# Kernel optimization log

Hardware: AMD Instinct MI355X
Metric: run time of the kernel (lower is better)

## Reference

```python
import jax, jax.numpy as jnp
import numpy as np

B, S, D, E, H, K = 2, 2048, 1024, 8, 2048, 2
EM_ITERS = 5
LB_WEIGHT = 0.1
EPS = 1e-8


def setup_inputs() -> dict:
    key = jax.random.key(0)
    ks = jax.random.split(key, 12)
    sc = 0.02
    return {
        "x": jax.random.normal(ks[0], (B, S, D), jnp.float32),
        "gate_W": jax.random.normal(ks[1], (D, E), jnp.float32) * sc,
        "gate_b": jnp.zeros((E,), jnp.float32),
        "gate_temp": jnp.ones((1,), jnp.float32),
        "W1": jax.random.normal(ks[2], (E, D, H), jnp.float32) * sc,
        "b1": jnp.zeros((E, H), jnp.float32),
        "W2": jax.random.normal(ks[3], (E, H, D), jnp.float32) * sc,
        "b2": jnp.zeros((E, D), jnp.float32),
        "sW1": jax.random.normal(ks[4], (D, H), jnp.float32) * sc,
        "sb1": jnp.zeros((H,), jnp.float32),
        "sW2": jax.random.normal(ks[5], (H, D), jnp.float32) * sc,
        "sb2": jnp.zeros((D,), jnp.float32),
    }


def reference(x, gate_W, gate_b, gate_temp, W1, b1, W2, b2, sW1, sb1, sW2, sb2):
    Bq, Sq, Dq = x.shape
    T = Bq * Sq
    xf = x.reshape(T, Dq)  # (T, D)

    # Router: gate linear + learned temperature
    gate_logits = xf @ gate_W + gate_b              # (T, E)
    tempered = gate_logits / gate_temp               # (T, E)
    expert_weights = jax.nn.softmax(tempered, axis=-1)
    _, topk_idx = jax.lax.top_k(expert_weights, K)   # (T, K) int32
    first = topk_idx[:, 0]

    # Load-balance loss: KL(uniform || empirical top-1 usage) (fresh counters)
    usage = jnp.zeros((E,), jnp.float32).at[first].add(1.0)
    actual = usage / jnp.float32(T)
    actual = actual + EPS
    actual = actual / actual.sum()
    u = jnp.float32(1.0 / E)
    kl = jnp.sum(u * (jnp.log(u) - jnp.log(actual)))
    load_balance_loss = LB_WEIGHT * kl

    # EM expert-load reweighting on tempered logits
    scores = jax.nn.softmax(tempered, axis=-1)       # (T, E)
    p = jnp.full((E,), 1.0 / E, jnp.float32)
    for _ in range(EM_ITERS):
        ea = scores * p                               # (T, E)
        ea = ea / (ea.sum(axis=-1, keepdims=True) + EPS)
        counts = ea.sum(axis=0)                       # (E,)
        p = counts / (counts.sum() + EPS)
    balanced = scores * p                             # (T, E)

    # All-expert FFN (dense, equivalent to per-expert masked compute)
    h = jax.nn.relu(jnp.einsum('td,edh->teh', xf, W1) + b1)  # (T, E, H)
    eo = jnp.einsum('teh,ehd->ted', h, W2) + b2              # (T, E, D)

    # Combine top-k experts with balanced weights
    w_k = jnp.take_along_axis(balanced, topk_idx, axis=1)        # (T, K)
    out_k = jnp.take_along_axis(eo, topk_idx[:, :, None], axis=1)  # (T, K, D)
    out = jnp.einsum('tk,tkd->td', w_k, out_k)                   # (T, D)

    # Shared expert, weighted by 0.1
    shared = jax.nn.relu(xf @ sW1 + sb1) @ sW2 + sb2
    out = out + 0.1 * shared

    return out.reshape(Bq, Sq, Dq), load_balance_loss
```

## Files before the change

### kernel.cpp

```cpp
#include <hip/hip_runtime.h>
#include <math.h>

#define T_TOK 4096
#define D_DIM 1024
#define H_DIM 2048
#define NE 8
#define EPSF 1e-8f
#define G1_GEMM 448
#define G2_GEMM 224
#define NTR128 1152

typedef __attribute__((ext_vector_type(8))) short bf16x8;
typedef __attribute__((ext_vector_type(4))) float f32x4;

__device__ __forceinline__ unsigned short f2bf(float f) {
  unsigned u = __float_as_uint(f);
  u += 0x7fffu + ((u >> 16) & 1u);
  return (unsigned short)(u >> 16);
}

__device__ __forceinline__ void gload_lds16(const void* g, void* l) {
  __builtin_amdgcn_global_load_lds(
      (const __attribute__((address_space(1))) unsigned int*)g,
      (__attribute__((address_space(3))) unsigned int*)l, 16, 0, 0);
}

#define WAITV(n) asm volatile("s_waitcnt vmcnt(" #n ")" ::: "memory")
#define BARR()                                  \
  do {                                          \
    asm volatile("" ::: "memory");              \
    __builtin_amdgcn_s_barrier();               \
    asm volatile("" ::: "memory");              \
  } while (0)

__device__ __forceinline__ void transpose_tile128(const float* __restrict__ src,
                                                  unsigned short* __restrict__ dst,
                                                  int R, int C, int r0, int c0, int tid,
                                                  float* tile) {
#pragma unroll
  for (int k = 0; k < 8; ++k) {
    int id = tid + k * 512;
    int row = id >> 5, c4 = (id & 31) * 4;
    float4 v = *(const float4*)(src + (size_t)(r0 + row) * C + c0 + c4);
    float* tr = tile + row * 129 + c4;
    tr[0] = v.x; tr[1] = v.y; tr[2] = v.z; tr[3] = v.w;
  }
  __syncthreads();
#pragma unroll
  for (int k = 0; k < 4; ++k) {
    int id = tid + k * 512;
    int oc = id >> 4;
    int rbase = (id & 15) * 8;
    uint4 wv;
    unsigned* wp = (unsigned*)&wv;
#pragma unroll
    for (int j = 0; j < 4; ++j) {
      unsigned lo = f2bf(tile[(rbase + 2 * j) * 129 + oc]);
      unsigned hi = f2bf(tile[(rbase + 2 * j + 1) * 129 + oc]);
      wp[j] = lo | (hi << 16);
    }
    *(uint4*)(dst + (size_t)(c0 + oc) * R + r0 + rbase) = wv;
  }
}

__global__ __launch_bounds__(512, 4) void gate_kernel(
    const float* __restrict__ x, const float* __restrict__ gW, const float* __restrict__ gb,
    const float* __restrict__ gtemp, unsigned short* __restrict__ xb,
    float* __restrict__ scores, int* __restrict__ idx,
    unsigned* __restrict__ usage, unsigned* __restrict__ cnt, int* __restrict__ perm) {
  __shared__ float gWl[D_DIM * 9];
  __shared__ int toks[16];
  int tid = threadIdx.x, wave = tid >> 6, lane = tid & 63;
  int t0 = blockIdx.x * 8;

#pragma unroll
  for (int k = 0; k < 4; ++k) {
    int q = tid + k * 512;
    float4 f = ((const float4*)gW)[q];
    int d = q >> 1, eo = (q & 1) * 4;
    float* dst = &gWl[d * 9 + eo];
    dst[0] = f.x; dst[1] = f.y; dst[2] = f.z; dst[3] = f.w;
  }
  __syncthreads();

  int t = t0 + wave;
  const float* xr = x + (size_t)t * D_DIM;
  unsigned short* xbr = xb + (size_t)t * D_DIM;
  float part[NE];
#pragma unroll
  for (int e = 0; e < NE; ++e) part[e] = 0.f;
#pragma unroll
  for (int i = 0; i < 16; ++i) {
    int d = lane + 64 * i;
    float xv = xr[d];
    xbr[d] = f2bf(xv);
    const float* g = &gWl[d * 9];
#pragma unroll
    for (int e = 0; e < NE; ++e) part[e] += xv * g[e];
  }
#pragma unroll
  for (int e = 0; e < NE; ++e) {
    float v = part[e];
    for (int off = 32; off; off >>= 1) v += __shfl_xor(v, off);
    part[e] = v;
  }
  float temp = gtemp[0];
  float mx = -1e30f;
#pragma unroll
  for (int e = 0; e < NE; ++e) { part[e] = (part[e] + gb[e]) / temp; mx = fmaxf(mx, part[e]); }
  float s = 0.f;
#pragma unroll
  for (int e = 0; e < NE; ++e) { part[e] = expf(part[e] - mx); s += part[e]; }
  float inv = 1.0f / s;
#pragma unroll
  for (int e = 0; e < NE; ++e) part[e] *= inv;
  if (lane == 0) {
    float4* sp = (float4*)(scores + (size_t)t * NE);
    sp[0] = make_float4(part[0], part[1], part[2], part[3]);
    sp[1] = make_float4(part[4], part[5], part[6], part[7]);
    int i0 = 0; float b0 = part[0];
#pragma unroll
    for (int e = 1; e < NE; ++e) if (part[e] > b0) { b0 = part[e]; i0 = e; }
    int i1 = -1; float b1 = -1e30f;
#pragma unroll
    for (int e = 0; e < NE; ++e) if (e != i0 && part[e] > b1) { b1 = part[e]; i1 = e; }
    idx[t * 2] = i0; idx[t * 2 + 1] = i1;
    toks[wave * 2] = i0; toks[wave * 2 + 1] = i1;
  }
  __syncthreads();
  if (tid < NE) {
    int c0 = 0, c1 = 0;
#pragma unroll
    for (int j = 0; j < 8; ++j) {
      if (toks[j * 2] == tid) ++c0;
      if (toks[j * 2 + 1] == tid) ++c1;
    }
    if (c0) atomicAdd(&usage[tid], (unsigned)c0);
    int tot = c0 + c1;
    if (tot) {
      unsigned b = atomicAdd(&cnt[tid], (unsigned)tot);
      int p = 0;
#pragma unroll
      for (int j = 0; j < 8; ++j) {
        if (toks[j * 2] == tid) perm[(size_t)tid * T_TOK + b + p++] = (t0 + j) * 2;
        if (toks[j * 2 + 1] == tid) perm[(size_t)tid * T_TOK + b + p++] = (t0 + j) * 2 + 1;
      }
    }
  }
}

__global__ __launch_bounds__(512) void transW1_kernel(
    const float* __restrict__ W1, const float* __restrict__ sW1,
    unsigned short* __restrict__ W1t, unsigned short* __restrict__ sW1t) {
  __shared__ float tile[128 * 129];
  int l = blockIdx.x;
  int m = l >> 7, rem = l & 127;
  int c0 = (rem & 15) * 128, r0 = (rem >> 4) * 128;
  const float* src = (m < NE) ? W1 + (size_t)m * D_DIM * H_DIM : sW1;
  unsigned short* dst = (m < NE) ? W1t + (size_t)m * D_DIM * H_DIM : sW1t;
  transpose_tile128(src, dst, D_DIM, H_DIM, r0, c0, threadIdx.x, tile);
}

__device__ __forceinline__ void em_block512(const float* __restrict__ scores,
                                            const unsigned* __restrict__ usage,
                                            float* __restrict__ p_out, float* __restrict__ loss_out,
                                            int tid, char* smem) {
  float* p_sh = (float*)smem;
  float* cw = p_sh + 8;
  float* counts_sh = cw + 64;
  int wave = tid >> 6, lane = tid & 63;
  float s[8][NE];
#pragma unroll
  for (int rr = 0; rr < 8; ++rr) {
    int row = tid + rr * 512;
    const float4* sp = (const float4*)(scores + (size_t)row * NE);
    float4 a = sp[0], b = sp[1];
    s[rr][0] = a.x; s[rr][1] = a.y; s[rr][2] = a.z; s[rr][3] = a.w;
    s[rr][4] = b.x; s[rr][5] = b.y; s[rr][6] = b.z; s[rr][7] = b.w;
  }
  if (tid < NE) p_sh[tid] = 1.0f / NE;
  __syncthreads();
  for (int it = 0; it < 5; ++it) {
    float p[NE];
#pragma unroll
    for (int e = 0; e < NE; ++e) p[e] = p_sh[e];
    float c[NE];
#pragma unroll
    for (int e = 0; e < NE; ++e) c[e] = 0.f;
#pragma unroll
    for (int rr = 0; rr < 8; ++rr) {
      float denom = 0.f;
#pragma unroll
      for (int e = 0; e < NE; ++e) denom += s[rr][e] * p[e];
      float inv = 1.0f / (denom + EPSF);
#pragma unroll
      for (int e = 0; e < NE; ++e) c[e] += s[rr][e] * p[e] * inv;
    }
#pragma unroll
    for (int e = 0; e < NE; ++e) {
      float v = c[e];
      for (int off = 32; off; off >>= 1) v += __shfl_xor(v, off);
      c[e] = v;
    }
    if (lane == 0) {
#pragma unroll
      for (int e = 0; e < NE; ++e) cw[wave * 8 + e] = c[e];
    }
    __syncthreads();
    if (tid < NE) {
      float tot = 0.f;
#pragma unroll
      for (int w = 0; w < 8; ++w) tot += cw[w * 8 + tid];
      counts_sh[tid] = tot;
    }
    __syncthreads();
    if (tid < NE) {
      float total = 0.f;
#pragma unroll
      for (int e = 0; e < NE; ++e) total += counts_sh[e];
      p_sh[tid] = counts_sh[tid] / (total + EPSF);
    }
    __syncthreads();
  }
  if (tid < NE) p_out[tid] = p_sh[tid];
  if (tid == 0) {
    float actual[NE]; float norm = 0.f;
#pragma unroll
    for (int e = 0; e < NE; ++e) { actual[e] = (float)usage[e] / (float)T_TOK + EPSF; norm += actual[e]; }
    float u = 1.0f / NE;
    float kl = 0.f;
#pragma unroll
    for (int e = 0; e < NE; ++e) kl += u * (logf(u) - logf(actual[e] / norm));
    loss_out[0] = 0.1f * kl;
  }
}

template <int KDIM, int NDIM, bool RELU, bool MODE1>
__device__ __forceinline__ void gemm_body(
    unsigned short* lds, int flat,
    const unsigned short* __restrict__ A, const unsigned short* __restrict__ WE,
    const unsigned short* __restrict__ WS, const float* __restrict__ biasE,
    const float* __restrict__ biasS, const int* __restrict__ perm,
    const unsigned* __restrict__ cnt, void* __restrict__ outp) {
  constexpr int BM = 256, BN = 256, BK = 64;
  constexpr int NT = NDIM / BN;
  constexpr int NKT = KDIM / BK;

  int tc[9];
#pragma unroll
  for (int i = 0; i < NE; ++i) tc[i] = ((int)cnt[i] + 255) >> 8;
  tc[8] = T_TOK / 256;
  int nt = 0;
#pragma unroll
  for (int i = 0; i < 9; ++i) nt += tc[i];
  int W = nt * NT;
  int xcd = flat & 7, pos = flat >> 3;
  int q = W >> 3, r = W & 7;
  int mycount = q + (xcd < r ? 1 : 0);
  if (pos >= mycount) return;
  int mystart = xcd * q + (xcd < r ? xcd : r);
  int w = mystart + pos;
  int ti = w / NT;
  int n0 = (w % NT) * BN;
  int e = 0, mt = ti;
  while (mt >= tc[e]) { mt -= tc[e]; ++e; }
  int m0 = mt * BM;
  int cnt_e = (e == NE) ? T_TOK : (int)cnt[e];

  const unsigned short* Bmat = (e == NE) ? WS : WE + (size_t)e * KDIM * NDIM;
  const float* bias = (e == NE) ? biasS : biasE + (size_t)e * NDIM;

  int tid = threadIdx.x, wave = tid >> 6, lane = tid & 63;
  int wm = wave >> 1, wn = wave & 1;
  int frow = lane & 15, fks = lane >> 4;

  int srow = wave * 8 + (lane >> 3);
  int sslot = lane & 7;
  const unsigned short* aptr[2][2];
  const unsigned short* bptr[2][2];
#pragma unroll
  for (int h = 0; h < 2; ++h)
#pragma unroll
    for (int j = 0; j < 2; ++j) {
      int rr = h * 128 + j * 64 + srow;
      int colsw = (sslot ^ (rr & 7)) << 3;
      int ar = m0 + rr;
      if (ar > cnt_e - 1) ar = cnt_e - 1;
      int gar;
      if (e == NE) gar = MODE1 ? ar : (2 * T_TOK + ar);
      else { int v = perm[(size_t)e * T_TOK + ar]; gar = MODE1 ? (v >> 1) : v; }
      aptr[h][j] = A + (size_t)gar * KDIM + colsw;
      bptr[h][j] = Bmat + (size_t)(n0 + rr) * KDIM + colsw;
    }

  auto stA = [&](int t, int h) {
    int dbe = (t & 1) * 16384;
    int k0 = t * BK;
    gload_lds16(aptr[h][0] + k0, &lds[dbe + h * 8192 + wave * 512]);
    gload_lds16(aptr[h][1] + k0, &lds[dbe + h * 8192 + wave * 512 + 4096]);
  };
  auto stB = [&](int t, int h) {
    int dbe = (t & 1) * 16384;
    int k0 = t * BK;
    gload_lds16(bptr[h][0] + k0, &lds[32768 + dbe + h * 8192 + wave * 512]);
    gload_lds16(bptr[h][1] + k0, &lds[32768 + dbe + h * 8192 + wave * 512 + 4096]);
  };

  auto rdA = [&](int dbe, int ks, int m) -> bf16x8 {
    int rr = wm * 64 + m * 16 + frow;
    int slot = (ks * 4 + fks) ^ (rr & 7);
    return *(const bf16x8*)&lds[dbe + rr * 64 + slot * 8];
  };
  auto rdB = [&](int dbe, int ks, int bh, int jj) -> bf16x8 {
    int rr = bh * 128 + jj * 32 + wn * 16 + frow;
    int slot = (ks * 4 + fks) ^ (rr & 7);
    return *(const bf16x8*)&lds[32768 + dbe + rr * 64 + slot * 8];
  };

  f32x4 acc[4][8];
#pragma unroll
  for (int m = 0; m < 4; ++m)
#pragma unroll
    for (int nn = 0; nn < 8; ++nn) acc[m][nn] = (f32x4){0.f, 0.f, 0.f, 0.f};

  stA(0, 0); stA(0, 1);
  stB(0, 0); stB(0, 1);
  stA(1, 0); stA(1, 1);
  WAITV(6);
  BARR();

  for (int t = 0; t < NKT; ++t) {
    const int dbe = (t & 1) * 16384;
    bf16x8 a0[4], a1[4], bfr[4];

#pragma unroll
    for (int m = 0; m < 4; ++m) a0[m] = rdA(dbe, 0, m);
#pragma unroll
    for (int jj = 0; jj < 4; ++jj) bfr[jj] = rdB(dbe, 0, 0, jj);
    if (t + 1 < NKT) stB(t + 1, 0);
    BARR();
    __builtin_amdgcn_s_setprio(1);
#pragma unroll
    for (int m = 0; m < 4; ++m)
#pragma unroll
      for (int jj = 0; jj < 4; ++jj)
        acc[m][jj] = __builtin_amdgcn_mfma_f32_16x16x32_bf16(a0[m], bfr[jj], acc[m][jj], 0, 0, 0);
    __builtin_amdgcn_s_setprio(0);
    BARR();

#pragma unroll
    for (int m = 0; m < 4; ++m) a1[m] = rdA(dbe, 1, m);
#pragma unroll
    for (int jj = 0; jj < 4; ++jj) bfr[jj] = rdB(dbe, 1, 0, jj);
    if (t + 1 < NKT) stB(t + 1, 1);
    BARR();
    __builtin_amdgcn_s_setprio(1);
#pragma unroll
    for (int m = 0; m < 4; ++m)
#pragma unroll
      for (int jj = 0; jj < 4; ++jj)
        acc[m][jj] = __builtin_amdgcn_mfma_f32_16x16x32_bf16(a1[m], bfr[jj], acc[m][jj], 0, 0, 0);
    __builtin_amdgcn_s_setprio(0);
    if (t + 1 < NKT) { WAITV(8); } else { WAITV(0); }
    BARR();

#pragma unroll
    for (int jj = 0; jj < 4; ++jj) bfr[jj] = rdB(dbe, 0, 1, jj);
    if (t + 2 < NKT) stA(t + 2, 0);
    BARR();
    __builtin_amdgcn_s_setprio(1);
#pragma unroll
    for (int m = 0; m < 4; ++m)
#pragma unroll
      for (int jj = 0; jj < 4; ++jj)
        acc[m][4 + jj] = __builtin_amdgcn_mfma_f32_16x16x32_bf16(a0[m], bfr[jj], acc[m][4 + jj], 0, 0, 0);
    __builtin_amdgcn_s_setprio(0);
    BARR();

#pragma unroll
    for (int jj = 0; jj < 4; ++jj) bfr[jj] = rdB(dbe, 1, 1, jj);
    if (t + 2 < NKT) stA(t + 2, 1);
    BARR();
    __builtin_amdgcn_s_setprio(1);
#pragma unroll
    for (int m = 0; m < 4; ++m)
#pragma unroll
      for (int jj = 0; jj < 4; ++jj)
        acc[m][4 + jj] = __builtin_amdgcn_mfma_f32_16x16x32_bf16(a1[m], bfr[jj], acc[m][4 + jj], 0, 0, 0);
    __builtin_amdgcn_s_setprio(0);
    if (t + 1 < NKT) {
      if (t + 2 < NKT) { WAITV(6); } else { WAITV(2); }
    }
    BARR();
  }

#pragma unroll
  for (int m = 0; m < 4; ++m) {
#pragma unroll
    for (int qq = 0; qq < 4; ++qq) {
      int rt = wm * 64 + m * 16 + (lane >> 4) * 4 + qq;
      if (m0 + rt >= cnt_e) continue;
      int rr;
      if (e == NE) rr = 2 * T_TOK + m0 + rt;
      else rr = perm[(size_t)e * T_TOK + m0 + rt];
#pragma unroll
      for (int nn = 0; nn < 8; ++nn) {
        int col = n0 + (nn >> 2) * 128 + (nn & 3) * 32 + wn * 16 + (lane & 15);
        float val = acc[m][nn][qq] + bias[col];
        if (RELU) val = fmaxf(val, 0.f);
        if (MODE1)
          ((unsigned short*)outp)[(size_t)rr * NDIM + col] = f2bf(val);
        else
          ((float*)outp)[(size_t)rr * NDIM + col] = val;
      }
    }
  }
}

__global__ __launch_bounds__(512, 2) void gemm1_kernel(
    const unsigned short* __restrict__ xb, const unsigned short* __restrict__ W1t,
    const unsigned short* __restrict__ sW1t, const float* __restrict__ b1,
    const float* __restrict__ sb1, const int* __restrict__ perm, const unsigned* __restrict__ cnt,
    unsigned short* __restrict__ Hbuf,
    const float* __restrict__ W2, const float* __restrict__ sW2,
    unsigned short* __restrict__ W2t, unsigned short* __restrict__ sW2t,
    const float* __restrict__ scores, const unsigned* __restrict__ usage,
    float* __restrict__ pbuf, float* __restrict__ loss_out) {
  __shared__ char smem[131072];
  int flat = blockIdx.x;
  if (flat < G1_GEMM) {
    gemm_body<D_DIM, H_DIM, true, true>((unsigned short*)smem, flat, xb, W1t, sW1t, b1, sb1,
                                        perm, cnt, (void*)Hbuf);
    return;
  }
  int l = flat - G1_GEMM;
  if (l < NTR128) {
    int m = l >> 7, rem = l & 127;
    int c0 = (rem & 7) * 128, r0 = (rem >> 3) * 128;
    const float* src = (m < NE) ? W2 + (size_t)m * H_DIM * D_DIM : sW2;
    unsigned short* dst = (m < NE) ? W2t + (size_t)m * H_DIM * D_DIM : sW2t;
    transpose_tile128(src, dst, H_DIM, D_DIM, r0, c0, threadIdx.x, (float*)smem);
    return;
  }
  em_block512(scores, usage, pbuf, loss_out, threadIdx.x, smem);
}

template <int KDIM, int NDIM, bool RELU, bool MODE1>
__global__ __launch_bounds__(512, 2) void gemm_kernel(
    const unsigned short* __restrict__ A, const unsigned short* __restrict__ WE,
    const unsigned short* __restrict__ WS, const float* __restrict__ biasE,
    const float* __restrict__ biasS, const int* __restrict__ perm,
    const unsigned* __restrict__ cnt, void* __restrict__ outp) {
  __shared__ char smem[131072];
  gemm_body<KDIM, NDIM, RELU, MODE1>((unsigned short*)smem, blockIdx.x, A, WE, WS, biasE, biasS,
                                     perm, cnt, outp);
}

__global__ void combine_kernel(const float* __restrict__ ebuf, const float* __restrict__ scores,
                               const float* __restrict__ p, const int* __restrict__ idx,
                               float* __restrict__ out) {
  int gid = blockIdx.x * blockDim.x + threadIdx.x;
  int t = gid >> 8;
  int d4 = gid & 255;
  int e0 = idx[t * 2], e1 = idx[t * 2 + 1];
  float w0 = scores[(size_t)t * NE + e0] * p[e0];
  float w1 = scores[(size_t)t * NE + e1] * p[e1];
  const float4* r0 = (const float4*)(ebuf + (size_t)(t * 2) * D_DIM);
  const float4* r1 = (const float4*)(ebuf + (size_t)(t * 2 + 1) * D_DIM);
  const float4* rs = (const float4*)(ebuf + (size_t)(2 * T_TOK + t) * D_DIM);
  float4 a = r0[d4], b = r1[d4], c = rs[d4];
  float4 o;
  o.x = w0 * a.x + w1 * b.x + 0.1f * c.x;
  o.y = w0 * a.y + w1 * b.y + 0.1f * c.y;
  o.z = w0 * a.z + w1 * b.z + 0.1f * c.z;
  o.w = w0 * a.w + w1 * b.w + 0.1f * c.w;
  ((float4*)out)[gid] = o;
}

extern "C" void kernel_launch(void* const* d_in, const int* in_sizes, int n_in,
                              void* d_out, int out_size, void* d_ws, size_t ws_size,
                              hipStream_t stream) {
  const float* x     = (const float*)d_in[0];
  const float* gW    = (const float*)d_in[1];
  const float* gb    = (const float*)d_in[2];
  const float* gtemp = (const float*)d_in[3];
  const float* W1    = (const float*)d_in[4];
  const float* b1    = (const float*)d_in[5];
  const float* W2    = (const float*)d_in[6];
  const float* b2    = (const float*)d_in[7];
  const float* sW1   = (const float*)d_in[8];
  const float* sb1   = (const float*)d_in[9];
  const float* sW2   = (const float*)d_in[10];
  const float* sb2   = (const float*)d_in[11];
  float* out = (float*)d_out;

  char* ws = (char*)d_ws;
  size_t off = 0;
  auto take = [&](size_t b) { char* ptr = ws + off; off += (b + 255) & ~(size_t)255; return ptr; };
  unsigned short* xb   = (unsigned short*)take((size_t)T_TOK * D_DIM * 2);
  unsigned short* W1t  = (unsigned short*)take((size_t)NE * H_DIM * D_DIM * 2);
  unsigned short* sW1t = (unsigned short*)take((size_t)H_DIM * D_DIM * 2);
  unsigned short* W2t  = (unsigned short*)take((size_t)NE * D_DIM * H_DIM * 2);
  unsigned short* sW2t = (unsigned short*)take((size_t)D_DIM * H_DIM * 2);
  unsigned short* Hbuf = (unsigned short*)take((size_t)3 * T_TOK * H_DIM * 2);
  float* ebuf          = (float*)take((size_t)3 * T_TOK * D_DIM * 4);
  float* scores        = (float*)take((size_t)T_TOK * NE * 4);
  int* idx             = (int*)take((size_t)T_TOK * 2 * 4);
  int* perm            = (int*)take((size_t)NE * T_TOK * 4);
  unsigned* cnt        = (unsigned*)take(256);
  unsigned* usage      = (unsigned*)take(256);
  float* pbuf          = (float*)take(256);
  (void)n_in; (void)in_sizes; (void)out_size; (void)ws_size;

  hipMemsetAsync(cnt, 0, 512, stream);
  gate_kernel<<<512, 512, 0, stream>>>(x, gW, gb, gtemp, xb, scores, idx, usage, cnt, perm);
  transW1_kernel<<<NTR128, 512, 0, stream>>>(W1, sW1, W1t, sW1t);
  gemm1_kernel<<<G1_GEMM + NTR128 + 1, 512, 0, stream>>>(
      xb, W1t, sW1t, b1, sb1, perm, cnt, Hbuf, W2, sW2, W2t, sW2t, scores, usage, pbuf,
      out + (size_t)T_TOK * D_DIM);
  gemm_kernel<H_DIM, D_DIM, false, false><<<G2_GEMM, 512, 0, stream>>>(
      Hbuf, W2t, sW2t, b2, sb2, perm, cnt, (void*)ebuf);
  combine_kernel<<<(T_TOK * D_DIM / 4) / 256, 256, 0, stream>>>(ebuf, scores, pbuf, idx, out);
}
```

Baseline: 198.0 us.

## Shrink GEMM tiles to 256x128x32 with triple-buffered A and fuse gate with W1 transpose

```diff
diff --git a/kernel.cpp b/kernel.cpp
--- a/kernel.cpp
+++ b/kernel.cpp
@@ -6,8 +6,8 @@
 #define H_DIM 2048
 #define NE 8
 #define EPSF 1e-8f
-#define G1_GEMM 448
-#define G2_GEMM 224
+#define G1_GEMM 896
+#define G2_GEMM 448
 #define NTR128 1152
 
 typedef __attribute__((ext_vector_type(8))) short bf16x8;
@@ -63,26 +63,36 @@
   }
 }
 
-__global__ __launch_bounds__(512, 4) void gate_kernel(
+__global__ __launch_bounds__(512, 4) void prep2_kernel(
     const float* __restrict__ x, const float* __restrict__ gW, const float* __restrict__ gb,
-    const float* __restrict__ gtemp, unsigned short* __restrict__ xb,
-    float* __restrict__ scores, int* __restrict__ idx,
+    const float* __restrict__ gtemp, const float* __restrict__ W1, const float* __restrict__ sW1,
+    unsigned short* __restrict__ W1t, unsigned short* __restrict__ sW1t,
+    unsigned short* __restrict__ xb, float* __restrict__ scores, int* __restrict__ idx,
     unsigned* __restrict__ usage, unsigned* __restrict__ cnt, int* __restrict__ perm) {
-  __shared__ float gWl[D_DIM * 9];
-  __shared__ int toks[16];
-  int tid = threadIdx.x, wave = tid >> 6, lane = tid & 63;
-  int t0 = blockIdx.x * 8;
-
+  __shared__ char psm[67584];
+  int b = blockIdx.x, tid = threadIdx.x;
+  if (b >= 512) {
+    int l = b - 512;
+    int m = l >> 7, rem = l & 127;
+    int c0 = (rem & 15) * 128, r0 = (rem >> 4) * 128;
+    const float* src = (m < NE) ? W1 + (size_t)m * D_DIM * H_DIM : sW1;
+    unsigned short* dst = (m < NE) ? W1t + (size_t)m * D_DIM * H_DIM : sW1t;
+    transpose_tile128(src, dst, D_DIM, H_DIM, r0, c0, tid, (float*)psm);
+    return;
+  }
+  float* gWl = (float*)psm;
+  int* toks = (int*)(psm + 36864);
+  int wave = tid >> 6, lane = tid & 63;
+  int t0 = b * 8;
 #pragma unroll
   for (int k = 0; k < 4; ++k) {
     int q = tid + k * 512;
     float4 f = ((const float4*)gW)[q];
     int d = q >> 1, eo = (q & 1) * 4;
-    float* dst = &gWl[d * 9 + eo];
-    dst[0] = f.x; dst[1] = f.y; dst[2] = f.z; dst[3] = f.w;
+    float* dstv = &gWl[d * 9 + eo];
+    dstv[0] = f.x; dstv[1] = f.y; dstv[2] = f.z; dstv[3] = f.w;
   }
   __syncthreads();
-
   int t = t0 + wave;
   const float* xr = x + (size_t)t * D_DIM;
   unsigned short* xbr = xb + (size_t)t * D_DIM;
@@ -138,27 +148,15 @@
     if (c0) atomicAdd(&usage[tid], (unsigned)c0);
     int tot = c0 + c1;
     if (tot) {
-      unsigned b = atomicAdd(&cnt[tid], (unsigned)tot);
+      unsigned bb = atomicAdd(&cnt[tid], (unsigned)tot);
       int p = 0;
 #pragma unroll
       for (int j = 0; j < 8; ++j) {
-        if (toks[j * 2] == tid) perm[(size_t)tid * T_TOK + b + p++] = (t0 + j) * 2;
-        if (toks[j * 2 + 1] == tid) perm[(size_t)tid * T_TOK + b + p++] = (t0 + j) * 2 + 1;
+        if (toks[j * 2] == tid) perm[(size_t)tid * T_TOK + bb + p++] = (t0 + j) * 2;
+        if (toks[j * 2 + 1] == tid) perm[(size_t)tid * T_TOK + bb + p++] = (t0 + j) * 2 + 1;
       }
     }
   }
-}
-
-__global__ __launch_bounds__(512) void transW1_kernel(
-    const float* __restrict__ W1, const float* __restrict__ sW1,
-    unsigned short* __restrict__ W1t, unsigned short* __restrict__ sW1t) {
-  __shared__ float tile[128 * 129];
-  int l = blockIdx.x;
-  int m = l >> 7, rem = l & 127;
-  int c0 = (rem & 15) * 128, r0 = (rem >> 4) * 128;
-  const float* src = (m < NE) ? W1 + (size_t)m * D_DIM * H_DIM : sW1;
-  unsigned short* dst = (m < NE) ? W1t + (size_t)m * D_DIM * H_DIM : sW1t;
-  transpose_tile128(src, dst, D_DIM, H_DIM, r0, c0, threadIdx.x, tile);
 }
 
 __device__ __forceinline__ void em_block512(const float* __restrict__ scores,
@@ -242,7 +240,7 @@
     const unsigned short* __restrict__ WS, const float* __restrict__ biasE,
     const float* __restrict__ biasS, const int* __restrict__ perm,
     const unsigned* __restrict__ cnt, void* __restrict__ outp) {
-  constexpr int BM = 256, BN = 256, BK = 64;
+  constexpr int BM = 256, BN = 128, BK = 32;
   constexpr int NT = NDIM / BN;
   constexpr int NKT = KDIM / BK;
 
@@ -274,124 +272,75 @@
   int wm = wave >> 1, wn = wave & 1;
   int frow = lane & 15, fks = lane >> 4;
 
-  int srow = wave * 8 + (lane >> 3);
-  int sslot = lane & 7;
-  const unsigned short* aptr[2][2];
-  const unsigned short* bptr[2][2];
-#pragma unroll
-  for (int h = 0; h < 2; ++h)
-#pragma unroll
-    for (int j = 0; j < 2; ++j) {
-      int rr = h * 128 + j * 64 + srow;
-      int colsw = (sslot ^ (rr & 7)) << 3;
-      int ar = m0 + rr;
-      if (ar > cnt_e - 1) ar = cnt_e - 1;
-      int gar;
-      if (e == NE) gar = MODE1 ? ar : (2 * T_TOK + ar);
-      else { int v = perm[(size_t)e * T_TOK + ar]; gar = MODE1 ? (v >> 1) : v; }
-      aptr[h][j] = A + (size_t)gar * KDIM + colsw;
-      bptr[h][j] = Bmat + (size_t)(n0 + rr) * KDIM + colsw;
-    }
-
-  auto stA = [&](int t, int h) {
-    int dbe = (t & 1) * 16384;
-    int k0 = t * BK;
-    gload_lds16(aptr[h][0] + k0, &lds[dbe + h * 8192 + wave * 512]);
-    gload_lds16(aptr[h][1] + k0, &lds[dbe + h * 8192 + wave * 512 + 4096]);
+  auto garf = [&](int rrow) {
+    int ar = m0 + rrow; if (ar > cnt_e - 1) ar = cnt_e - 1;
+    int gar;
+    if (e == NE) gar = MODE1 ? ar : (2 * T_TOK + ar);
+    else { int v = perm[(size_t)e * T_TOK + ar]; gar = MODE1 ? (v >> 1) : v; }
+    return gar;
   };
-  auto stB = [&](int t, int h) {
-    int dbe = (t & 1) * 16384;
-    int k0 = t * BK;
-    gload_lds16(bptr[h][0] + k0, &lds[32768 + dbe + h * 8192 + wave * 512]);
-    gload_lds16(bptr[h][1] + k0, &lds[32768 + dbe + h * 8192 + wave * 512 + 4096]);
+  int r0a = wave * 16 + (lane >> 2);
+  int r1a = 128 + wave * 16 + (lane >> 2);
+  int rb = wave * 16 + (lane >> 2);
+  int g0 = (r0a & 3) ^ ((r0a >> 2) & 3);
+  int g1 = (r1a & 3) ^ ((r1a >> 2) & 3);
+  int gbv = (rb & 3) ^ ((rb >> 2) & 3);
+  const unsigned short* aptr0 = A + (size_t)garf(r0a) * KDIM + (((lane & 3) ^ g0) << 3);
+  const unsigned short* aptr1 = A + (size_t)garf(r1a) * KDIM + (((lane & 3) ^ g1) << 3);
+  const unsigned short* bptr = Bmat + (size_t)(n0 + rb) * KDIM + (((lane & 3) ^ gbv) << 3);
+
+  auto stA = [&](int t, int ab) {
+    gload_lds16(aptr0 + t * BK, &lds[ab * 8192 + wave * 512]);
+    gload_lds16(aptr1 + t * BK, &lds[ab * 8192 + 4096 + wave * 512]);
   };
-
-  auto rdA = [&](int dbe, int ks, int m) -> bf16x8 {
+  auto stB = [&](int t) {
+    gload_lds16(bptr + t * BK, &lds[24576 + (t & 1) * 4096 + wave * 512]);
+  };
+
+  auto rdA = [&](int ab, int m) -> bf16x8 {
     int rr = wm * 64 + m * 16 + frow;
-    int slot = (ks * 4 + fks) ^ (rr & 7);
-    return *(const bf16x8*)&lds[dbe + rr * 64 + slot * 8];
+    int sp = fks ^ ((rr & 3) ^ ((rr >> 2) & 3));
+    return *(const bf16x8*)&lds[ab * 8192 + rr * 32 + sp * 8];
   };
-  auto rdB = [&](int dbe, int ks, int bh, int jj) -> bf16x8 {
-    int rr = bh * 128 + jj * 32 + wn * 16 + frow;
-    int slot = (ks * 4 + fks) ^ (rr & 7);
-    return *(const bf16x8*)&lds[32768 + dbe + rr * 64 + slot * 8];
+  auto rdB = [&](int bb, int j) -> bf16x8 {
+    int rr = wn * 64 + j * 16 + frow;
+    int sp = fks ^ ((rr & 3) ^ ((rr >> 2) & 3));
+    return *(const bf16x8*)&lds[24576 + bb * 4096 + rr * 32 + sp * 8];
   };
 
-  f32x4 acc[4][8];
+  f32x4 acc[4][4];
 #pragma unroll
   for (int m = 0; m < 4; ++m)
 #pragma unroll
-    for (int nn = 0; nn < 8; ++nn) acc[m][nn] = (f32x4){0.f, 0.f, 0.f, 0.f};
-
-  stA(0, 0); stA(0, 1);
-  stB(0, 0); stB(0, 1);
-  stA(1, 0); stA(1, 1);
-  WAITV(6);
+    for (int j = 0; j < 4; ++j) acc[m][j] = (f32x4){0.f, 0.f, 0.f, 0.f};
+
+  stA(0, 0); stB(0); stA(1, 1);
+  WAITV(2);
   BARR();
 
+  int ab = 0;
   for (int t = 0; t < NKT; ++t) {
-    const int dbe = (t & 1) * 16384;
-    bf16x8 a0[4], a1[4], bfr[4];
-
-#pragma unroll
-    for (int m = 0; m < 4; ++m) a0[m] = rdA(dbe, 0, m);
-#pragma unroll
-    for (int jj = 0; jj < 4; ++jj) bfr[jj] = rdB(dbe, 0, 0, jj);
-    if (t + 1 < NKT) stB(t + 1, 0);
+    int bb = t & 1;
+    bf16x8 a[4], b[4];
+#pragma unroll
+    for (int m = 0; m < 4; ++m) a[m] = rdA(ab, m);
+#pragma unroll
+    for (int j = 0; j < 4; ++j) b[j] = rdB(bb, j);
+    if (t + 1 < NKT) stB(t + 1);
+    if (t + 2 < NKT) { int ab2 = ab + 2; if (ab2 >= 3) ab2 -= 3; stA(t + 2, ab2); }
     BARR();
     __builtin_amdgcn_s_setprio(1);
 #pragma unroll
     for (int m = 0; m < 4; ++m)
 #pragma unroll
-      for (int jj = 0; jj < 4; ++jj)
-        acc[m][jj] = __builtin_amdgcn_mfma_f32_16x16x32_bf16(a0[m], bfr[jj], acc[m][jj], 0, 0, 0);
-    __builtin_amdgcn_s_setprio(0);
-    BARR();
-
-#pragma unroll
-    for (int m = 0; m < 4; ++m) a1[m] = rdA(dbe, 1, m);
-#pragma unroll
-    for (int jj = 0; jj < 4; ++jj) bfr[jj] = rdB(dbe, 1, 0, jj);
-    if (t + 1 < NKT) stB(t + 1, 1);
-    BARR();
-    __builtin_amdgcn_s_setprio(1);
-#pragma unroll
-    for (int m = 0; m < 4; ++m)
-#pragma unroll
-      for (int jj = 0; jj < 4; ++jj)
-        acc[m][jj] = __builtin_amdgcn_mfma_f32_16x16x32_bf16(a1[m], bfr[jj], acc[m][jj], 0, 0, 0);
-    __builtin_amdgcn_s_setprio(0);
-    if (t + 1 < NKT) { WAITV(8); } else { WAITV(0); }
-    BARR();
-
-#pragma unroll
-    for (int jj = 0; jj < 4; ++jj) bfr[jj] = rdB(dbe, 0, 1, jj);
-    if (t + 2 < NKT) stA(t + 2, 0);
-    BARR();
-    __builtin_amdgcn_s_setprio(1);
-#pragma unroll
-    for (int m = 0; m < 4; ++m)
-#pragma unroll
-      for (int jj = 0; jj < 4; ++jj)
-        acc[m][4 + jj] = __builtin_amdgcn_mfma_f32_16x16x32_bf16(a0[m], bfr[jj], acc[m][4 + jj], 0, 0, 0);
-    __builtin_amdgcn_s_setprio(0);
-    BARR();
-
-#pragma unroll
-    for (int jj = 0; jj < 4; ++jj) bfr[jj] = rdB(dbe, 1, 1, jj);
-    if (t + 2 < NKT) stA(t + 2, 1);
-    BARR();
-    __builtin_amdgcn_s_setprio(1);
-#pragma unroll
-    for (int m = 0; m < 4; ++m)
-#pragma unroll
-      for (int jj = 0; jj < 4; ++jj)
-        acc[m][4 + jj] = __builtin_amdgcn_mfma_f32_16x16x32_bf16(a1[m], bfr[jj], acc[m][4 + jj], 0, 0, 0);
+      for (int j = 0; j < 4; ++j)
+        acc[m][j] = __builtin_amdgcn_mfma_f32_16x16x32_bf16(a[m], b[j], acc[m][j], 0, 0, 0);
     __builtin_amdgcn_s_setprio(0);
     if (t + 1 < NKT) {
-      if (t + 2 < NKT) { WAITV(6); } else { WAITV(2); }
-    }
-    BARR();
+      if (t + 2 < NKT) { WAITV(2); } else { WAITV(0); }
+      BARR();
+    }
+    ab = (ab == 2) ? 0 : ab + 1;
   }
 
 #pragma unroll
@@ -404,9 +353,9 @@
       if (e == NE) rr = 2 * T_TOK + m0 + rt;
       else rr = perm[(size_t)e * T_TOK + m0 + rt];
 #pragma unroll
-      for (int nn = 0; nn < 8; ++nn) {
-        int col = n0 + (nn >> 2) * 128 + (nn & 3) * 32 + wn * 16 + (lane & 15);
-        float val = acc[m][nn][qq] + bias[col];
+      for (int j = 0; j < 4; ++j) {
+        int col = n0 + wn * 64 + j * 16 + (lane & 15);
+        float val = acc[m][j][qq] + bias[col];
         if (RELU) val = fmaxf(val, 0.f);
         if (MODE1)
           ((unsigned short*)outp)[(size_t)rr * NDIM + col] = f2bf(val);
@@ -417,7 +366,7 @@
   }
 }
 
-__global__ __launch_bounds__(512, 2) void gemm1_kernel(
+__global__ __launch_bounds__(512, 4) void gemm1_kernel(
     const unsigned short* __restrict__ xb, const unsigned short* __restrict__ W1t,
     const unsigned short* __restrict__ sW1t, const float* __restrict__ b1,
     const float* __restrict__ sb1, const int* __restrict__ perm, const unsigned* __restrict__ cnt,
@@ -426,7 +375,7 @@
     unsigned short* __restrict__ W2t, unsigned short* __restrict__ sW2t,
     const float* __restrict__ scores, const unsigned* __restrict__ usage,
     float* __restrict__ pbuf, float* __restrict__ loss_out) {
-  __shared__ char smem[131072];
+  __shared__ char smem[67584];
   int flat = blockIdx.x;
   if (flat < G1_GEMM) {
     gemm_body<D_DIM, H_DIM, true, true>((unsigned short*)smem, flat, xb, W1t, sW1t, b1, sb1,
@@ -446,12 +395,12 @@
 }
 
 template <int KDIM, int NDIM, bool RELU, bool MODE1>
-__global__ __launch_bounds__(512, 2) void gemm_kernel(
+__global__ __launch_bounds__(512, 4) void gemm_kernel(
     const unsigned short* __restrict__ A, const unsigned short* __restrict__ WE,
     const unsigned short* __restrict__ WS, const float* __restrict__ biasE,
     const float* __restrict__ biasS, const int* __restrict__ perm,
     const unsigned* __restrict__ cnt, void* __restrict__ outp) {
-  __shared__ char smem[131072];
+  __shared__ char smem[67584];
   gemm_body<KDIM, NDIM, RELU, MODE1>((unsigned short*)smem, blockIdx.x, A, WE, WS, biasE, biasS,
                                      perm, cnt, outp);
 }
@@ -513,8 +462,8 @@
   (void)n_in; (void)in_sizes; (void)out_size; (void)ws_size;
 
   hipMemsetAsync(cnt, 0, 512, stream);
-  gate_kernel<<<512, 512, 0, stream>>>(x, gW, gb, gtemp, xb, scores, idx, usage, cnt, perm);
-  transW1_kernel<<<NTR128, 512, 0, stream>>>(W1, sW1, W1t, sW1t);
+  prep2_kernel<<<512 + NTR128, 512, 0, stream>>>(x, gW, gb, gtemp, W1, sW1, W1t, sW1t, xb,
+                                                 scores, idx, usage, cnt, perm);
   gemm1_kernel<<<G1_GEMM + NTR128 + 1, 512, 0, stream>>>(
       xb, W1t, sW1t, b1, sb1, perm, cnt, Hbuf, W2, sW2, W2t, sW2t, scores, usage, pbuf,
       out + (size_t)T_TOK * D_DIM);
```

Measured after the change: 203.5 us. 2.8% more time.
